# Performance work log

Measured on AMD Instinct MI355X. Metric: run time of the kernel, lower is better.

The kernel has to match this reference:

```python
import jax, jax.numpy as jnp
import numpy as np

def setup_inputs() -> dict:
    key = jax.random.key(0)
    k1, k2, k3, k4 = jax.random.split(key, 4)
    B = 128
    x1 = jax.random.normal(k1, (B, 2048, 7, 7), dtype=jnp.float32)
    x2 = jax.random.normal(k2, (B, 2048, 7, 7), dtype=jnp.float32)
    x3 = jax.random.normal(k3, (B, 2048, 7, 7), dtype=jnp.float32)
    W = jax.random.normal(k4, (14, 2048), dtype=jnp.float32) * 0.02
    b = jnp.zeros((14,), dtype=jnp.float32)
    return {"x1": x1, "x2": x2, "x3": x3, "W": W, "b": b}

def reference(x1, x2, x3, W, b):
    B = x1.shape[0]
    # (B, 2048, 49)
    x1r = x1.reshape(B, 2048, 49)
    x2r = x2.reshape(B, 2048, 49)
    x3r = x3.reshape(B, 2048, 49)
    # diagonal of matmul(x3, x1^T) == per-row dot product over the 49-dim axis
    # (avoids materializing the (B,2048,2048) intermediate)
    d31 = jnp.einsum('bnc,bnc->bn', x3r, x1r)[..., None]  # (B, 2048, 1)
    d32 = jnp.einsum('bnc,bnc->bn', x3r, x2r)[..., None]
    # softmax over last (singleton) axis -> all ones, kept for faithfulness
    d31 = jax.nn.softmax(d31, axis=-1)
    d32 = jax.nn.softmax(d32, axis=-1)
    h = x1r + x1r * d31 + x2r * d32  # (B, 2048, 49)
    # AvgPool2d(7) on (B,2048,7,7) == mean over the 49 spatial positions
    feats = jnp.mean(h, axis=-1)  # (B, 2048)
    # dropout omitted (deterministic eval); fc
    logits = feats @ W.T + b  # (B, 14)
    return (logits, feats)
```

## Files before the change

### kernel.cpp

```cpp
#include <hip/hip_runtime.h>


#define NROWS (128 * 2048)
#define FC_B 128
#define FC_N 2048
#define FC_J 14
#define RPB 64
#define NBLK (NROWS / RPB)
#define BPB (FC_N / RPB)

__global__ __launch_bounds__(1024) void fused_kernel(const float* __restrict__ x1,
                                                     const float* __restrict__ x2,
                                                     const float* __restrict__ W,
                                                     float* __restrict__ feats,
                                                     float* __restrict__ part) {
    const int tid = threadIdx.x;
    const int g = tid >> 4;
    const int t = tid & 15;
    const int r = blockIdx.x * RPB + g;

    const float* p1 = x1 + (size_t)r * 49;
    const float* p2 = x2 + (size_t)r * 49;

    float a = p1[t] + p1[t + 16] + p1[t + 32];
    float c = p2[t] + p2[t + 16] + p2[t + 32];
    if (t == 0) { a += p1[48]; c += p2[48]; }
    float v = 2.0f * a + c;

    #pragma unroll
    for (int m = 8; m >= 1; m >>= 1)
        v += __shfl_xor(v, m, 16);

    __shared__ float sf[RPB];
    if (t == 0) {
        const float fv = v * (1.0f / 49.0f);
        feats[r] = fv;
        sf[g] = fv;
    }
    __syncthreads();

    if (tid < FC_J) {
        const int n0 = (blockIdx.x & (BPB - 1)) * RPB;
        const float* wrow = W + tid * FC_N + n0;
        float acc = 0.0f;
        #pragma unroll
        for (int k = 0; k < RPB; ++k)
            acc += sf[k] * wrow[k];
        part[blockIdx.x * FC_J + tid] = acc;
    }
}

__global__ __launch_bounds__(256) void gather_kernel(const float* __restrict__ part,
                                                     const float* __restrict__ bias,
                                                     float* __restrict__ logits) {
    const int idx = blockIdx.x * 256 + threadIdx.x;
    if (idx >= FC_B * FC_J) return;
    const int b = idx / FC_J;
    const int j = idx % FC_J;
    float s = bias[j];
    #pragma unroll
    for (int i = 0; i < BPB; ++i)
        s += part[(size_t)(b * BPB + i) * FC_J + j];
    logits[idx] = s;
}

extern "C" void kernel_launch(void* const* d_in, const int* in_sizes, int n_in,
                              void* d_out, int out_size, void* d_ws, size_t ws_size,
                              hipStream_t stream) {
    const float* x1 = (const float*)d_in[0];
    const float* x2 = (const float*)d_in[1];
    const float* W = (const float*)d_in[3];
    const float* bias = (const float*)d_in[4];

    float* out = (float*)d_out;
    float* logits = out;
    float* feats = out + FC_B * FC_J;

    float* part = (float*)d_ws;

    fused_kernel<<<NBLK, 1024, 0, stream>>>(x1, x2, W, feats, part);
    gather_kernel<<<(FC_B * FC_J + 255) / 256, 256, 0, stream>>>(part, bias, logits);
}
```

Before: 26.10 us.

## Process multiple rows per thread group and fuse FC accumulation into loop

Each 256-thread block now handles 128 rows over an unrolled loop of 8 iterations per 16-lane group. Each lane accumulates its FC output column directly as row means are produced, replacing the serial shared-memory dot product done by only 14 threads. The aim is more independent loads in flight, less serial tail work per block, and fewer partial sums for the gather kernel. It may raise register pressure and reduce the number of blocks available for latency hiding.

```diff
diff --git a/kernel.cpp b/kernel.cpp
--- a/kernel.cpp
+++ b/kernel.cpp
@@ -5,48 +5,54 @@
 #define FC_B 128
 #define FC_N 2048
 #define FC_J 14
-#define RPB 64
-#define NBLK (NROWS / RPB)
-#define BPB (FC_N / RPB)
+#define GROUPS 16
+#define ITERS 8
+#define ROWS_PER_BLOCK (GROUPS * ITERS)
+#define NBLK (NROWS / ROWS_PER_BLOCK)
+#define BLK_PER_B (FC_N / ROWS_PER_BLOCK)
 
-__global__ __launch_bounds__(1024) void fused_kernel(const float* __restrict__ x1,
-                                                     const float* __restrict__ x2,
-                                                     const float* __restrict__ W,
-                                                     float* __restrict__ feats,
-                                                     float* __restrict__ part) {
+__global__ __launch_bounds__(256, 8) void fused_kernel(const float* __restrict__ x1,
+                                                       const float* __restrict__ x2,
+                                                       const float* __restrict__ W,
+                                                       float* __restrict__ feats,
+                                                       float* __restrict__ part) {
     const int tid = threadIdx.x;
     const int g = tid >> 4;
     const int t = tid & 15;
-    const int r = blockIdx.x * RPB + g;
+    const int rbase = blockIdx.x * ROWS_PER_BLOCK;
 
-    const float* p1 = x1 + (size_t)r * 49;
-    const float* p2 = x2 + (size_t)r * 49;
-
-    float a = p1[t] + p1[t + 16] + p1[t + 32];
-    float c = p2[t] + p2[t + 16] + p2[t + 32];
-    if (t == 0) { a += p1[48]; c += p2[48]; }
-    float v = 2.0f * a + c;
+    const float* wrow = W + (t < FC_J ? t : 0) * FC_N;
+    float accj = 0.0f;
 
     #pragma unroll
-    for (int m = 8; m >= 1; m >>= 1)
-        v += __shfl_xor(v, m, 16);
+    for (int it = 0; it < ITERS; ++it) {
+        const int r = rbase + it * GROUPS + g;
+        const float* p1 = x1 + (size_t)r * 49;
+        const float* p2 = x2 + (size_t)r * 49;
 
-    __shared__ float sf[RPB];
-    if (t == 0) {
+        float a = p1[t] + p1[t + 16] + p1[t + 32];
+        float c = p2[t] + p2[t + 16] + p2[t + 32];
+        if (t == 0) { a += p1[48]; c += p2[48]; }
+        float v = 2.0f * a + c;
+
+        #pragma unroll
+        for (int m = 8; m >= 1; m >>= 1)
+            v += __shfl_xor(v, m, 16);
+
         const float fv = v * (1.0f / 49.0f);
-        feats[r] = fv;
-        sf[g] = fv;
+        if (t == 0) feats[r] = fv;
+        if (t < FC_J) accj += fv * wrow[r & (FC_N - 1)];
     }
+
+    __shared__ float sp[GROUPS][FC_J];
+    if (t < FC_J) sp[g][t] = accj;
     __syncthreads();
 
     if (tid < FC_J) {
-        const int n0 = (blockIdx.x & (BPB - 1)) * RPB;
-        const float* wrow = W + tid * FC_N + n0;
-        float acc = 0.0f;
+        float s = 0.0f;
         #pragma unroll
-        for (int k = 0; k < RPB; ++k)
-            acc += sf[k] * wrow[k];
-        part[blockIdx.x * FC_J + tid] = acc;
+        for (int k = 0; k < GROUPS; ++k) s += sp[k][tid];
+        part[blockIdx.x * FC_J + tid] = s;
     }
 }
 
@@ -59,8 +65,8 @@
     const int j = idx % FC_J;
     float s = bias[j];
     #pragma unroll
-    for (int i = 0; i < BPB; ++i)
-        s += part[(size_t)(b * BPB + i) * FC_J + j];
+    for (int i = 0; i < BLK_PER_B; ++i)
+        s += part[(size_t)(b * BLK_PER_B + i) * FC_J + j];
     logits[idx] = s;
 }
 
@@ -78,6 +84,6 @@
 
     float* part = (float*)d_ws;
 
-    fused_kernel<<<NBLK, 1024, 0, stream>>>(x1, x2, W, feats, part);
+    fused_kernel<<<NBLK, 256, 0, stream>>>(x1, x2, W, feats, part);
     gather_kernel<<<(FC_B * FC_J + 255) / 256, 256, 0, stream>>>(part, bias, logits);
 }
```

Result: faster. 24.05 us (-7.8%).

## Assign two rows per thread with float2 loads and restructure FC partials

Applied to the files above, without the earlier changes.

The row reduction moves from 16 threads per row with shuffles to one thread handling two consecutive rows (98 floats) through float2 loads. The grid drops to 512 blocks of 256 threads. The FC partial is now computed by 224 threads with a shuffle reduction, and the partials are laid out so the gather kernel reads one float4 per logit. The per-thread strided access is uncoalesced across lanes and leaves far fewer threads to hide memory latency, which risks lower bandwidth on a memory-bound reduction.

```diff
diff --git a/kernel.cpp b/kernel.cpp
--- a/kernel.cpp
+++ b/kernel.cpp
@@ -5,48 +5,67 @@
 #define FC_B 128
 #define FC_N 2048
 #define FC_J 14
-#define RPB 64
-#define NBLK (NROWS / RPB)
-#define BPB (FC_N / RPB)
+#define NBLK 512
+#define QPB 4
 
-__global__ __launch_bounds__(1024) void fused_kernel(const float* __restrict__ x1,
-                                                     const float* __restrict__ x2,
-                                                     const float* __restrict__ W,
-                                                     float* __restrict__ feats,
-                                                     float* __restrict__ part) {
+__global__ __launch_bounds__(256) void fused_kernel(
+    const float* __restrict__ x1, const float* __restrict__ x2,
+    const float* __restrict__ W,
+    float* __restrict__ feats, float* __restrict__ part)
+{
     const int tid = threadIdx.x;
-    const int g = tid >> 4;
-    const int t = tid & 15;
-    const int r = blockIdx.x * RPB + g;
+    const size_t T = (size_t)blockIdx.x * 256 + tid;
+    const float2* q1 = (const float2*)x1 + T * 49;
+    const float2* q2 = (const float2*)x2 + T * 49;
 
-    const float* p1 = x1 + (size_t)r * 49;
-    const float* p2 = x2 + (size_t)r * 49;
-
-    float a = p1[t] + p1[t + 16] + p1[t + 32];
-    float c = p2[t] + p2[t + 16] + p2[t + 32];
-    if (t == 0) { a += p1[48]; c += p2[48]; }
-    float v = 2.0f * a + c;
+    float s1A = 0.f, s1B = 0.f, s2A = 0.f, s2B = 0.f;
 
     #pragma unroll
-    for (int m = 8; m >= 1; m >>= 1)
-        v += __shfl_xor(v, m, 16);
+    for (int m = 0; m < 24; ++m) {
+        const float2 a = q1[m];
+        const float2 c = q2[m];
+        s1A += a.x + a.y;
+        s2A += c.x + c.y;
+    }
+    {
+        const float2 a = q1[24];
+        const float2 c = q2[24];
+        s1A += a.x;  s1B += a.y;
+        s2A += c.x;  s2B += c.y;
+    }
+    #pragma unroll
+    for (int m = 25; m < 49; ++m) {
+        const float2 a = q1[m];
+        const float2 c = q2[m];
+        s1B += a.x + a.y;
+        s2B += c.x + c.y;
+    }
 
-    __shared__ float sf[RPB];
-    if (t == 0) {
-        const float fv = v * (1.0f / 49.0f);
-        feats[r] = fv;
-        sf[g] = fv;
-    }
+    float2 fv;
+    fv.x = (2.0f * s1A + s2A) * (1.0f / 49.0f);
+    fv.y = (2.0f * s1B + s2B) * (1.0f / 49.0f);
+    ((float2*)feats)[T] = fv;
+
+    __shared__ float sf[512];
+    ((float2*)sf)[tid] = fv;
     __syncthreads();
 
-    if (tid < FC_J) {
-        const int n0 = (blockIdx.x & (BPB - 1)) * RPB;
-        const float* wrow = W + tid * FC_N + n0;
+    if (tid < 224) {
+        const int j = tid >> 4;
+        const int s = tid & 15;
+        const int bb = blockIdx.x >> 2;
+        const int q  = blockIdx.x & (QPB - 1);
+        const float* wrow = W + j * FC_N + q * 512;
         float acc = 0.0f;
         #pragma unroll
-        for (int k = 0; k < RPB; ++k)
-            acc += sf[k] * wrow[k];
-        part[blockIdx.x * FC_J + tid] = acc;
+        for (int k = 0; k < 32; ++k)
+            acc += sf[s + 16 * k] * wrow[s + 16 * k];
+        acc += __shfl_xor(acc, 1, 16);
+        acc += __shfl_xor(acc, 2, 16);
+        acc += __shfl_xor(acc, 4, 16);
+        acc += __shfl_xor(acc, 8, 16);
+        if (s == 0)
+            part[((bb * FC_J + j) << 2) + q] = acc;
     }
 }
 
@@ -55,13 +74,8 @@
                                                      float* __restrict__ logits) {
     const int idx = blockIdx.x * 256 + threadIdx.x;
     if (idx >= FC_B * FC_J) return;
-    const int b = idx / FC_J;
-    const int j = idx % FC_J;
-    float s = bias[j];
-    #pragma unroll
-    for (int i = 0; i < BPB; ++i)
-        s += part[(size_t)(b * BPB + i) * FC_J + j];
-    logits[idx] = s;
+    const float4 p = *(const float4*)(part + ((size_t)idx << 2));
+    logits[idx] = p.x + p.y + p.z + p.w + bias[idx % FC_J];
 }
 
 extern "C" void kernel_launch(void* const* d_in, const int* in_sizes, int n_in,
@@ -78,6 +92,6 @@
 
     float* part = (float*)d_ws;
 
-    fused_kernel<<<NBLK, 1024, 0, stream>>>(x1, x2, W, feats, part);
+    fused_kernel<<<NBLK, 256, 0, stream>>>(x1, x2, W, feats, part);
     gather_kernel<<<(FC_B * FC_J + 255) / 256, 256, 0, stream>>>(part, bias, logits);
 }
```

Result: slower. 49.96 us (+91.4%).
